# Kernel optimization log

Measured on AMD Instinct MI355X. Metric: run time of the kernel, lower is better.

## Reference

```python
import jax, jax.numpy as jnp
import numpy as np

P = 16  # patch size
D = 768  # embedding dim


def setup_inputs() -> dict:
    key = jax.random.key(0)
    k_img, k_w, k_b = jax.random.split(key, 3)
    B, H, W, C = 64, 224, 224, 3
    image = jax.random.normal(k_img, (B, H, W, C), dtype=jnp.float32)
    patch_dim = P * P * C  # 768
    # Keras Dense default: glorot_uniform kernel, zeros bias
    limit = np.sqrt(6.0 / (patch_dim + D)).astype(np.float32)
    W_proj = jax.random.uniform(k_w, (patch_dim, D), dtype=jnp.float32,
                                minval=-limit, maxval=limit)
    b_proj = jnp.zeros((D,), dtype=jnp.float32)
    return {"image": image, "W_proj": W_proj, "b_proj": b_proj}


def reference(image, W_proj, b_proj):
    B, H, W, C = image.shape
    nh, nw = H // P, W // P
    # Fused im2col replacing the per-patch slicing loop:
    # [B,H,W,C] -> [B, nh, P, nw, P, C] -> [B, nh, nw, P, P, C] -> [B, nh*nw, P*P*C]
    # Row-major (p_i, p_j) patch order matches the original nested loop, and
    # flatten of a [B,P,P,C] slice matches the (P,P,C) raveling here.
    patches = image.reshape(B, nh, P, nw, P, C)
    patches = patches.transpose(0, 1, 3, 2, 4, 5).reshape(B, nh * nw, P * P * C)
    # Dense + exact GELU (tf.keras.activations.gelu default approximate=False)
    x = jnp.einsum('bnp,pd->bnd', patches, W_proj) + b_proj
    return jax.nn.gelu(x, approximate=False)
```

## Files before the change

kernel.cpp:

```cpp
#include <hip/hip_runtime.h>
#include <hip/hip_bf16.h>
#include <math.h>

#define MM 12544
#define KK 768
#define NN 768
#define BM 64
#define BN 256
#define BK 64
#define KT 12
#define MT 196
#define NT 3
#define TILE_B_BYTES (BN*BK*2)

#define WTPACK_BLOCKS ((NN * 96) / 256)

typedef __bf16 v8bf __attribute__((ext_vector_type(8)));
typedef float  v4f  __attribute__((ext_vector_type(4)));

__global__ __launch_bounds__(256) void wt_pack(const float* __restrict__ w,
                                               __hip_bfloat16* __restrict__ wpack) {
    int tid = blockIdx.x * 256 + threadIdx.x;
    int n   = tid % 768;
    int gg  = tid / 768;
    int k0  = gg * 8;
    float f[8];
#pragma unroll
    for (int j = 0; j < 8; j++) f[j] = w[(size_t)(k0 + j) * NN + n];
    int nt = n >> 8;
    int nr = n & 255;
    int kt = gg >> 3;
    int g  = gg & 7;
    int gs = g ^ (nr & 7);
    union { __hip_bfloat16 h[8]; uint4 u; } o;
#pragma unroll
    for (int j = 0; j < 8; j++) o.h[j] = __float2bfloat16(f[j]);
    *(uint4*)(wpack + ((size_t)(nt * KT + kt) * BN + nr) * BK + gs * 8) = o.u;
}

__device__ __forceinline__ float gelu_fast(float x) {
    float t2 = 1.5957691216057308f * x * (1.0f + 0.044715f * x * x);
    float e  = __expf(t2);
    float r  = __builtin_amdgcn_rcpf(e + 1.0f);
    return x - x * r;
}

__global__ __launch_bounds__(256, 3) void gemm_gelu(const float* __restrict__ img,
                                                    const __hip_bfloat16* __restrict__ wpack,
                                                    const float* __restrict__ bias,
                                                    float* __restrict__ out) {
    __shared__ __align__(16) __hip_bfloat16 As[BM * BK];
    __shared__ __align__(16) __hip_bfloat16 Bs[BN * BK];

    const int blk = blockIdx.x;
    const int nt  = blk % 3;
    const int mt  = blk / 3;

    const int tid  = threadIdx.x;
    const int lane = tid & 63;
    const int wave = tid >> 6;
    const int wn   = wave * 64;
    const int col  = lane & 15;
    const int quad = lane >> 4;
    const int cl7  = col & 7;

    const int r = tid >> 2;
    const int q = tid & 3;
    unsigned m  = (unsigned)(mt * BM + r);
    unsigned b  = m / 196u;
    unsigned pm = m - b * 196u;
    unsigned pr = pm / 14u;
    unsigned pc = pm - pr * 14u;
    const float* pbase = img + (size_t)(((b * 224u + pr * 16u) * 224u + pc * 16u) * 3u);
    const int gs0 = (2 * q) ^ (r & 7);
    const int gs1 = gs0 ^ 1;
    uint4* As16 = (uint4*)As;

    v4f acc[4][4];
    const v4f vzero = {0.f, 0.f, 0.f, 0.f};
#pragma unroll
    for (int a = 0; a < 4; a++)
#pragma unroll
        for (int c = 0; c < 4; c++) acc[a][c] = vzero;

    const char* bT = (const char*)wpack + (size_t)nt * KT * TILE_B_BYTES;

    for (int kt = 0; kt < KT; kt++) {
#pragma unroll
        for (int p = 0; p < 8; p++) {
            int off = p * 4096 + tid * 16;
            __builtin_amdgcn_global_load_lds(
                (const __attribute__((address_space(1))) void*)(bT + off),
                (__attribute__((address_space(3))) void*)((char*)Bs + off), 16, 0, 0);
        }
        bT += TILE_B_BYTES;

        float4 f4[4];
#pragma unroll
        for (int j = 0; j < 4; j++) {
            unsigned k   = (unsigned)(kt * 64 + q * 16 + j * 4);
            unsigned i   = k / 48u;
            unsigned rem = k - i * 48u;
            f4[j] = *(const float4*)(pbase + i * 672u + rem);
        }
        union { __hip_bfloat16 h[8]; uint4 u; } lo, hi;
        lo.h[0] = __float2bfloat16(f4[0].x); lo.h[1] = __float2bfloat16(f4[0].y);
        lo.h[2] = __float2bfloat16(f4[0].z); lo.h[3] = __float2bfloat16(f4[0].w);
        lo.h[4] = __float2bfloat16(f4[1].x); lo.h[5] = __float2bfloat16(f4[1].y);
        lo.h[6] = __float2bfloat16(f4[1].z); lo.h[7] = __float2bfloat16(f4[1].w);
        hi.h[0] = __float2bfloat16(f4[2].x); hi.h[1] = __float2bfloat16(f4[2].y);
        hi.h[2] = __float2bfloat16(f4[2].z); hi.h[3] = __float2bfloat16(f4[2].w);
        hi.h[4] = __float2bfloat16(f4[3].x); hi.h[5] = __float2bfloat16(f4[3].y);
        hi.h[6] = __float2bfloat16(f4[3].z); hi.h[7] = __float2bfloat16(f4[3].w);
        As16[r * 8 + gs0] = lo.u;
        As16[r * 8 + gs1] = hi.u;

        __syncthreads();

#pragma unroll
        for (int ks = 0; ks < 2; ks++) {
            const int gs = (ks * 4 + quad) ^ cl7;
            const v8bf* pa = (const v8bf*)(As + col * BK + gs * 8);
            const v8bf* pb = (const v8bf*)(Bs + (wn + col) * BK + gs * 8);
            v8bf af[4], bfr[4];
#pragma unroll
            for (int mi = 0; mi < 4; mi++) af[mi] = pa[mi * 128];
#pragma unroll
            for (int ni = 0; ni < 4; ni++) bfr[ni] = pb[ni * 128];
#pragma unroll
            for (int mi = 0; mi < 4; mi++)
#pragma unroll
                for (int ni = 0; ni < 4; ni++)
                    acc[mi][ni] = __builtin_amdgcn_mfma_f32_16x16x32_bf16(
                        af[mi], bfr[ni], acc[mi][ni], 0, 0, 0);
        }
        __syncthreads();
    }

#pragma unroll
    for (int ni = 0; ni < 4; ni++) {
        int n    = nt * BN + wn + ni * 16 + col;
        float bv = bias[n];
#pragma unroll
        for (int mi = 0; mi < 4; mi++) {
            int rowb = mt * BM + mi * 16 + quad * 4;
            float* po = out + (size_t)rowb * NN + n;
#pragma unroll
            for (int rg = 0; rg < 4; rg++) {
                float x = acc[mi][ni][rg] + bv;
                po[(size_t)rg * NN] = gelu_fast(x);
            }
        }
    }
}

extern "C" void kernel_launch(void* const* d_in, const int* in_sizes, int n_in,
                              void* d_out, int out_size, void* d_ws, size_t ws_size,
                              hipStream_t stream) {
    const float* img   = (const float*)d_in[0];
    const float* wproj = (const float*)d_in[1];
    const float* bias  = (const float*)d_in[2];
    float* out = (float*)d_out;

    __hip_bfloat16* wpack = (__hip_bfloat16*)d_ws;

    wt_pack<<<dim3(WTPACK_BLOCKS), dim3(256), 0, stream>>>(wproj, wpack);
    gemm_gelu<<<dim3(MT * NT), dim3(256), 0, stream>>>(img, wpack, bias, out);
}
```

Measured before the change: 124.5 us.

## Double-buffer A and B shared-memory tiles to overlap loads with MFMA

Adds ping-pong LDS buffers for the A and B tiles. Tile k+1 is prefetched (direct global-to-LDS for B, register loads for A) while MFMAs run on tile k, and one barrier per iteration replaces two. This hides global memory latency behind compute. In exchange LDS use doubles to 80KB per block, and the occupancy hint drops from 3 to 2 blocks per CU.

New measurement: 130.8 us. 5.1% more time.

```diff
diff --git a/kernel.cpp b/kernel.cpp
--- a/kernel.cpp
+++ b/kernel.cpp
@@ -45,12 +45,12 @@
     return x - x * r;
 }
 
-__global__ __launch_bounds__(256, 3) void gemm_gelu(const float* __restrict__ img,
+__global__ __launch_bounds__(256, 2) void gemm_gelu(const float* __restrict__ img,
                                                     const __hip_bfloat16* __restrict__ wpack,
                                                     const float* __restrict__ bias,
                                                     float* __restrict__ out) {
-    __shared__ __align__(16) __hip_bfloat16 As[BM * BK];
-    __shared__ __align__(16) __hip_bfloat16 Bs[BN * BK];
+    __shared__ __align__(16) __hip_bfloat16 As[2 * BM * BK];
+    __shared__ __align__(16) __hip_bfloat16 Bs[2 * BN * BK];
 
     const int blk = blockIdx.x;
     const int nt  = blk % 3;
@@ -74,7 +74,6 @@
     const float* pbase = img + (size_t)(((b * 224u + pr * 16u) * 224u + pc * 16u) * 3u);
     const int gs0 = (2 * q) ^ (r & 7);
     const int gs1 = gs0 ^ 1;
-    uint4* As16 = (uint4*)As;
 
     v4f acc[4][4];
     const v4f vzero = {0.f, 0.f, 0.f, 0.f};
@@ -85,20 +84,18 @@
 
     const char* bT = (const char*)wpack + (size_t)nt * KT * TILE_B_BYTES;
 
-    for (int kt = 0; kt < KT; kt++) {
-#pragma unroll
-        for (int p = 0; p < 8; p++) {
-            int off = p * 4096 + tid * 16;
-            __builtin_amdgcn_global_load_lds(
-                (const __attribute__((address_space(1))) void*)(bT + off),
-                (__attribute__((address_space(3))) void*)((char*)Bs + off), 16, 0, 0);
-        }
-        bT += TILE_B_BYTES;
-
+#pragma unroll
+    for (int p = 0; p < 8; p++) {
+        int off = p * 4096 + tid * 16;
+        __builtin_amdgcn_global_load_lds(
+            (const __attribute__((address_space(1))) void*)(bT + off),
+            (__attribute__((address_space(3))) void*)((char*)Bs + off), 16, 0, 0);
+    }
+    {
         float4 f4[4];
 #pragma unroll
         for (int j = 0; j < 4; j++) {
-            unsigned k   = (unsigned)(kt * 64 + q * 16 + j * 4);
+            unsigned k   = (unsigned)(q * 16 + j * 4);
             unsigned i   = k / 48u;
             unsigned rem = k - i * 48u;
             f4[j] = *(const float4*)(pbase + i * 672u + rem);
@@ -112,16 +109,43 @@
         hi.h[2] = __float2bfloat16(f4[2].z); hi.h[3] = __float2bfloat16(f4[2].w);
         hi.h[4] = __float2bfloat16(f4[3].x); hi.h[5] = __float2bfloat16(f4[3].y);
         hi.h[6] = __float2bfloat16(f4[3].z); hi.h[7] = __float2bfloat16(f4[3].w);
+        uint4* As16 = (uint4*)As;
         As16[r * 8 + gs0] = lo.u;
         As16[r * 8 + gs1] = hi.u;
-
-        __syncthreads();
+    }
+    __syncthreads();
+
+    for (int kt = 0; kt < KT; kt++) {
+        const int cur = kt & 1;
+        const __hip_bfloat16* Asc = As + cur * (BM * BK);
+        const __hip_bfloat16* Bsc = Bs + cur * (BN * BK);
+
+        float4 f4[4];
+        const bool more = (kt + 1 < KT);
+        if (more) {
+            const char* bN  = bT + (size_t)(kt + 1) * TILE_B_BYTES;
+            char*       BsN = (char*)(Bs + (cur ^ 1) * (BN * BK));
+#pragma unroll
+            for (int p = 0; p < 8; p++) {
+                int off = p * 4096 + tid * 16;
+                __builtin_amdgcn_global_load_lds(
+                    (const __attribute__((address_space(1))) void*)(bN + off),
+                    (__attribute__((address_space(3))) void*)(BsN + off), 16, 0, 0);
+            }
+#pragma unroll
+            for (int j = 0; j < 4; j++) {
+                unsigned k   = (unsigned)((kt + 1) * 64 + q * 16 + j * 4);
+                unsigned i   = k / 48u;
+                unsigned rem = k - i * 48u;
+                f4[j] = *(const float4*)(pbase + i * 672u + rem);
+            }
+        }
 
 #pragma unroll
         for (int ks = 0; ks < 2; ks++) {
             const int gs = (ks * 4 + quad) ^ cl7;
-            const v8bf* pa = (const v8bf*)(As + col * BK + gs * 8);
-            const v8bf* pb = (const v8bf*)(Bs + (wn + col) * BK + gs * 8);
+            const v8bf* pa = (const v8bf*)(Asc + col * BK + gs * 8);
+            const v8bf* pb = (const v8bf*)(Bsc + (wn + col) * BK + gs * 8);
             v8bf af[4], bfr[4];
 #pragma unroll
             for (int mi = 0; mi < 4; mi++) af[mi] = pa[mi * 128];
@@ -133,6 +157,21 @@
                 for (int ni = 0; ni < 4; ni++)
                     acc[mi][ni] = __builtin_amdgcn_mfma_f32_16x16x32_bf16(
                         af[mi], bfr[ni], acc[mi][ni], 0, 0, 0);
+        }
+
+        if (more) {
+            union { __hip_bfloat16 h[8]; uint4 u; } lo, hi;
+            lo.h[0] = __float2bfloat16(f4[0].x); lo.h[1] = __float2bfloat16(f4[0].y);
+            lo.h[2] = __float2bfloat16(f4[0].z); lo.h[3] = __float2bfloat16(f4[0].w);
+            lo.h[4] = __float2bfloat16(f4[1].x); lo.h[5] = __float2bfloat16(f4[1].y);
+            lo.h[6] = __float2bfloat16(f4[1].z); lo.h[7] = __float2bfloat16(f4[1].w);
+            hi.h[0] = __float2bfloat16(f4[2].x); hi.h[1] = __float2bfloat16(f4[2].y);
+            hi.h[2] = __float2bfloat16(f4[2].z); hi.h[3] = __float2bfloat16(f4[2].w);
+            hi.h[4] = __float2bfloat16(f4[3].x); hi.h[5] = __float2bfloat16(f4[3].y);
+            hi.h[6] = __float2bfloat16(f4[3].z); hi.h[7] = __float2bfloat16(f4[3].w);
+            uint4* AsN = (uint4*)(As + (cur ^ 1) * (BM * BK));
+            AsN[r * 8 + gs0] = lo.u;
+            AsN[r * 8 + gs1] = hi.u;
         }
         __syncthreads();
     }
```
